# Kernel tuning notes

Measured on AMD Instinct MI355X. Metric: run time of the kernel, lower is better.

## Reference

```python
import jax, jax.numpy as jnp
import numpy as np

N_HEAD, D_K, D_V, EPS = 8, 64, 64, 1e-6


def setup_inputs() -> dict:
    key = jax.random.key(0)
    ks = jax.random.split(key, 7)
    b, n, t, d = 8, 4, 512, 512
    q = jax.random.normal(ks[0], (b, n, t, d), dtype=jnp.float32)
    k = jax.random.normal(ks[1], (b, n, t, d), dtype=jnp.float32)
    v = jax.random.normal(ks[2], (b, n, t, d), dtype=jnp.float32)
    s = 1.0 / np.sqrt(d)
    w_q = jax.random.normal(ks[3], (N_HEAD * D_K, d), dtype=jnp.float32) * s
    w_k = jax.random.normal(ks[4], (N_HEAD * D_K, d), dtype=jnp.float32) * s
    w_v = jax.random.normal(ks[5], (N_HEAD * D_V, d), dtype=jnp.float32) * s
    w_fc = jax.random.normal(ks[6], (d, N_HEAD * D_V), dtype=jnp.float32) * s
    ln_gamma = jnp.ones((d,), dtype=jnp.float32)
    ln_beta = jnp.zeros((d,), dtype=jnp.float32)
    return {"q": q, "k": k, "v": v, "w_q": w_q, "w_k": w_k, "w_v": w_v,
            "w_fc": w_fc, "ln_gamma": ln_gamma, "ln_beta": ln_beta}


def reference(q, k, v, w_q, w_k, w_v, w_fc, ln_gamma, ln_beta):
    b, n, t, d = q.shape
    B = b * n
    qf = q.reshape(B, t, d)
    kf = k.reshape(B, t, d)
    vf = v.reshape(B, t, d)
    residual = qf
    # projections -> [B, H, T, dk/dv]
    Q = jnp.einsum('btd,ed->bte', qf, w_q).reshape(B, t, N_HEAD, D_K).transpose(0, 2, 1, 3)
    K = jnp.einsum('btd,ed->bte', kf, w_k).reshape(B, t, N_HEAD, D_K).transpose(0, 2, 1, 3)
    V = jnp.einsum('btd,ed->bte', vf, w_v).reshape(B, t, N_HEAD, D_V).transpose(0, 2, 1, 3)
    # scaled dot-product attention (scale by sqrt(d_k) of q's last dim)
    scale = 1.0 / jnp.sqrt(jnp.asarray(D_K, dtype=Q.dtype))
    attn = jax.nn.softmax(jnp.einsum('bhqd,bhkd->bhqk', Q * scale, K), axis=-1)
    O = jnp.einsum('bhqk,bhkd->bhqd', attn, V)  # [B, H, T, dv]
    # merge heads, then the original's extra transpose+view (layout scramble)
    x = O.transpose(0, 2, 1, 3).reshape(B, t, N_HEAD * D_V)
    x = jnp.transpose(x, (0, 2, 1)).reshape(B, t, N_HEAD * D_V)
    x = jnp.einsum('bte,de->btd', x, w_fc)
    x = x + residual
    # LayerNorm(eps=1e-6)
    mu = jnp.mean(x, axis=-1, keepdims=True)
    var = jnp.var(x, axis=-1, keepdims=True)
    x = (x - mu) * jax.lax.rsqrt(var + EPS) * ln_gamma + ln_beta
    return x.reshape(b, n, t, d)
```

## Files before the change

### kernel.cpp

```cpp
#include <hip/hip_runtime.h>
#include <hip/hip_bf16.h>
#include <stdint.h>

typedef __attribute__((ext_vector_type(8))) short bf16x8;
typedef __attribute__((ext_vector_type(4))) float f32x4;
typedef unsigned int u32;

#define MFMA16(a,b,c) __builtin_amdgcn_mfma_f32_16x16x32_bf16((a),(b),(c),0,0,0)

__device__ __forceinline__ unsigned short f2bf(float f) {
    unsigned u = __float_as_uint(f);
    u = (u + 0x7FFFu + ((u >> 16) & 1u)) >> 16;
    return (unsigned short)u;
}
__device__ __forceinline__ float bf2f(unsigned short h) {
    return __uint_as_float(((unsigned)h) << 16);
}
__device__ __forceinline__ void gload16(const unsigned short* gp, unsigned short* lp) {
    __builtin_amdgcn_global_load_lds(
        (const __attribute__((address_space(1))) u32*)gp,
        (__attribute__((address_space(3))) u32*)lp, 16, 0, 0);
}
__device__ __forceinline__ int xcd_swz(int bid, int q8) {
    return (bid & 7) * q8 + (bid >> 3);
}


__global__ __launch_bounds__(256) void prep_kernel(
    const float* __restrict__ q, const float* __restrict__ k, const float* __restrict__ v,
    const float* __restrict__ wq, const float* __restrict__ wk, const float* __restrict__ wv,
    const float* __restrict__ wfc,
    unsigned short* __restrict__ Xq, unsigned short* __restrict__ Xk, unsigned short* __restrict__ Xv,
    unsigned short* __restrict__ Wcat)
{
    const long total = 3276800;
    for (long c = (long)blockIdx.x * 256 + threadIdx.x; c < total; c += (long)gridDim.x * 256) {
        const float* src;
        unsigned short* dst;
        long off;
        if (c < 3145728) {
            int t = (int)(c >> 20);
            off = (c & 1048575) * 8;
            src = (t == 0) ? q : (t == 1) ? k : v;
            dst = (t == 0) ? Xq : (t == 1) ? Xk : Xv;
        } else {
            long c2 = c - 3145728;
            int w = (int)(c2 >> 15);
            off = (c2 & 32767) * 8;
            src = (w == 0) ? wq : (w == 1) ? wk : (w == 2) ? wv : wfc;
            dst = Wcat + (long)w * 262144;
        }
        const float4 a = *(const float4*)(src + off);
        const float4 b = *(const float4*)(src + off + 4);
        uint4 pk;
        pk.x = (u32)f2bf(a.x) | ((u32)f2bf(a.y) << 16);
        pk.y = (u32)f2bf(a.z) | ((u32)f2bf(a.w) << 16);
        pk.z = (u32)f2bf(b.x) | ((u32)f2bf(b.y) << 16);
        pk.w = (u32)f2bf(b.z) | ((u32)f2bf(b.w) << 16);
        *(uint4*)(dst + off) = pk;
    }
}

__device__ __forceinline__ void gemm_body(
    const unsigned short* __restrict__ A, const unsigned short* __restrict__ Bm,
    unsigned short* __restrict__ out, int mode, float scale,
    unsigned short* As0, unsigned short* Bs0,
    unsigned short* As1, unsigned short* Bs1,
    int m0, int n0)
{
    const int tid = threadIdx.x, wid = tid >> 6, lane = tid & 63;
    const int wm = wid >> 1, wn = wid & 1;
    const int g = lane >> 4, cc = lane & 15;

    f32x4 acc[4][4];
    #pragma unroll
    for (int a = 0; a < 4; a++)
        #pragma unroll
        for (int b = 0; b < 4; b++)
            acc[a][b] = (f32x4){0.f, 0.f, 0.f, 0.f};

    auto STAGE = [&](unsigned short* As, unsigned short* Bs, int k0) {
        #pragma unroll
        for (int j = 0; j < 4; j++) {
            const int sb = j * 256 + wid * 64;
            const int s = sb + lane;
            const int r = s >> 3;
            const int cd = (s & 7) ^ (r & 7);
            gload16(A  + (size_t)(m0 + r) * 512 + k0 + cd * 8, As + (size_t)sb * 8);
            gload16(Bm + (size_t)(n0 + r) * 512 + k0 + cd * 8, Bs + (size_t)sb * 8);
        }
    };

    STAGE(As0, Bs0, 0);
    __syncthreads();

    #pragma unroll
    for (int t = 0; t < 8; t++) {
        unsigned short* Ac = (t & 1) ? As1 : As0;
        unsigned short* Bc = (t & 1) ? Bs1 : Bs0;
        if (t < 7)
            STAGE((t & 1) ? As0 : As1, (t & 1) ? Bs0 : Bs1, (t + 1) * 64);

        #pragma unroll
        for (int kc = 0; kc < 2; kc++) {
            bf16x8 af[4], bfr[4];
            #pragma unroll
            for (int mf = 0; mf < 4; mf++) {
                const int r = wm * 64 + mf * 16 + cc;
                af[mf] = *(const bf16x8*)(Ac + r * 64 + (((kc * 4 + g) ^ (r & 7)) * 8));
            }
            #pragma unroll
            for (int nf = 0; nf < 4; nf++) {
                const int r = wn * 64 + nf * 16 + cc;
                bfr[nf] = *(const bf16x8*)(Bc + r * 64 + (((kc * 4 + g) ^ (r & 7)) * 8));
            }
            __builtin_amdgcn_s_setprio(1);
            #pragma unroll
            for (int mf = 0; mf < 4; mf++)
                #pragma unroll
                for (int nf = 0; nf < 4; nf++)
                    acc[mf][nf] = MFMA16(af[mf], bfr[nf], acc[mf][nf]);
            __builtin_amdgcn_s_setprio(0);
        }
        __syncthreads();
    }

    #pragma unroll
    for (int mf = 0; mf < 4; mf++) {
        const int rg = m0 + wm * 64 + mf * 16 + g * 4;
        const int t0 = rg & 511, bI = rg >> 9;
        #pragma unroll
        for (int nf = 0; nf < 4; nf++) {
            const int col = n0 + wn * 64 + nf * 16 + cc;
            if (mode == 0) {
                const int h = col >> 6, dd = col & 63;
                const size_t base = ((size_t)((bI * 8 + h) * 512 + t0)) * 64 + dd;
                #pragma unroll
                for (int i = 0; i < 4; i++)
                    out[base + (size_t)i * 64] = f2bf(acc[mf][nf][i] * scale);
            } else if (mode == 1) {
                const int h = col >> 6, dd = col & 63;
                const size_t base = ((size_t)((bI * 8 + h) * 64 + dd)) * 512 + t0;
                uint2 pk;
                pk.x = (u32)f2bf(acc[mf][nf][0]) | ((u32)f2bf(acc[mf][nf][1]) << 16);
                pk.y = (u32)f2bf(acc[mf][nf][2]) | ((u32)f2bf(acc[mf][nf][3]) << 16);
                *(uint2*)(out + base) = pk;
            } else {
                #pragma unroll
                for (int i = 0; i < 4; i++)
                    out[(size_t)(rg + i) * 512 + col] = f2bf(acc[mf][nf][i]);
            }
        }
    }
}

__global__ __launch_bounds__(256) void proj_kernel(
    const unsigned short* __restrict__ Xq, const unsigned short* __restrict__ Xk,
    const unsigned short* __restrict__ Xv, const unsigned short* __restrict__ Wcat,
    unsigned short* __restrict__ Qb, unsigned short* __restrict__ Kb,
    unsigned short* __restrict__ Vt)
{
    __shared__ __align__(16) unsigned short As[2][128 * 64];
    __shared__ __align__(16) unsigned short Bs[2][128 * 64];
    const int work = xcd_swz(blockIdx.x, 192);
    const int x = work & 3, y = (work >> 2) & 127, z = work >> 9;
    const unsigned short* A = (z == 0) ? Xq : (z == 1) ? Xk : Xv;
    const unsigned short* B = Wcat + (size_t)z * 262144;
    unsigned short* out = (z == 0) ? Qb : (z == 1) ? Kb : Vt;
    const int mode = (z == 2) ? 1 : 0;
    const float scale = (z == 0) ? 0.125f : 1.0f;
    gemm_body(A, B, out, mode, scale, As[0], Bs[0], As[1], Bs[1], y * 128, x * 128);
}

__global__ __launch_bounds__(256) void fc_kernel(
    const unsigned short* __restrict__ Os, const unsigned short* __restrict__ Wfc,
    unsigned short* __restrict__ Y)
{
    __shared__ __align__(16) unsigned short As[2][128 * 64];
    __shared__ __align__(16) unsigned short Bs[2][128 * 64];
    const int work = xcd_swz(blockIdx.x, 64);
    const int x = work & 3, y = work >> 2;
    gemm_body(Os, Wfc, Y, 2, 1.0f, As[0], Bs[0], As[1], Bs[1], y * 128, x * 128);
}

__global__ __launch_bounds__(256) void attn_kernel(
    const unsigned short* __restrict__ Qb, const unsigned short* __restrict__ Kb,
    const unsigned short* __restrict__ Vt, unsigned short* __restrict__ Os)
{
    __shared__ __align__(16) unsigned short Ks[64 * 64];
    __shared__ __align__(16) unsigned short Vs[64 * 64];
    __shared__ __align__(16) unsigned short Ps[4 * 32 * 64];

    const int work = xcd_swz(blockIdx.x, 128);
    const int qt = work & 3, bh = work >> 2;
    const int tid = threadIdx.x;
    const int wid = tid >> 6, lane = tid & 63;
    const int g = lane >> 4, cc = lane & 15;

    const unsigned short* Qp = Qb + (size_t)bh * 512 * 64;
    const unsigned short* Kp = Kb + (size_t)bh * 512 * 64;
    const unsigned short* Vp = Vt + (size_t)bh * 64 * 512;

    const int q0 = qt * 128 + wid * 32;

    bf16x8 qf[2][2];
    #pragma unroll
    for (int mf = 0; mf < 2; mf++)
        #pragma unroll
        for (int kb = 0; kb < 2; kb++)
            qf[mf][kb] = *(const bf16x8*)(Qp + (size_t)(q0 + mf * 16 + cc) * 64 + kb * 32 + g * 8);

    f32x4 o[2][4];
    #pragma unroll
    for (int a = 0; a < 2; a++)
        #pragma unroll
        for (int b = 0; b < 4; b++)
            o[a][b] = (f32x4){0.f, 0.f, 0.f, 0.f};
    float lrun[2][4];
    #pragma unroll
    for (int a = 0; a < 2; a++)
        #pragma unroll
        for (int i = 0; i < 4; i++) lrun[a][i] = 0.f;

    const int sb = wid * 64;
    const int s1 = sb + lane, r1 = s1 >> 3, cd1 = (s1 & 7) ^ (r1 & 7);
    const int s2 = sb + 256 + lane, r2 = s2 >> 3, cd2 = (s2 & 7) ^ (r2 & 7);

    for (int kt = 0; kt < 8; kt++) {
        gload16(Kp + (size_t)(kt * 64 + r1) * 64 + cd1 * 8, Ks + (size_t)sb * 8);
        gload16(Kp + (size_t)(kt * 64 + r2) * 64 + cd2 * 8, Ks + (size_t)(sb + 256) * 8);
        gload16(Vp + (size_t)r1 * 512 + kt * 64 + cd1 * 8, Vs + (size_t)sb * 8);
        gload16(Vp + (size_t)r2 * 512 + kt * 64 + cd2 * 8, Vs + (size_t)(sb + 256) * 8);
        __syncthreads();

        f32x4 s[2][4];
        #pragma unroll
        for (int a = 0; a < 2; a++)
            #pragma unroll
            for (int b = 0; b < 4; b++)
                s[a][b] = (f32x4){0.f, 0.f, 0.f, 0.f};
        __builtin_amdgcn_s_setprio(1);
        #pragma unroll
        for (int nf = 0; nf < 4; nf++) {
            const int r = nf * 16 + cc;
            #pragma unroll
            for (int kb = 0; kb < 2; kb++) {
                bf16x8 kf = *(const bf16x8*)(Ks + r * 64 + (((kb * 4 + g) ^ (r & 7)) * 8));
                s[0][nf] = MFMA16(qf[0][kb], kf, s[0][nf]);
                s[1][nf] = MFMA16(qf[1][kb], kf, s[1][nf]);
            }
        }
        __builtin_amdgcn_s_setprio(0);

        unsigned short* Pw = Ps + wid * 32 * 64;
        #pragma unroll
        for (int mf = 0; mf < 2; mf++)
            #pragma unroll
            for (int i = 0; i < 4; i++) {
                float lacc = 0.f;
                #pragma unroll
                for (int nf = 0; nf < 4; nf++) {
                    float p = __expf(s[mf][nf][i]);
                    s[mf][nf][i] = p;
                    lacc += p;
                }
                lrun[mf][i] += lacc;
            }

        #pragma unroll
        for (int mf = 0; mf < 2; mf++)
            #pragma unroll
            for (int nf = 0; nf < 4; nf++) {
                const int c = nf * 16 + cc, csl = c >> 3, cin = c & 7;
                #pragma unroll
                for (int i = 0; i < 4; i++) {
                    const int row = mf * 16 + g * 4 + i;
                    Pw[row * 64 + ((csl ^ (row & 7)) * 8) + cin] = f2bf(s[mf][nf][i]);
                }
            }

        __builtin_amdgcn_s_setprio(1);
        #pragma unroll
        for (int kc = 0; kc < 2; kc++) {
            bf16x8 pa[2], vb[4];
            #pragma unroll
            for (int mf = 0; mf < 2; mf++) {
                const int r = mf * 16 + cc;
                pa[mf] = *(const bf16x8*)(Pw + r * 64 + (((kc * 4 + g) ^ (r & 7)) * 8));
            }
            #pragma unroll
            for (int vf = 0; vf < 4; vf++) {
                const int r = vf * 16 + cc;
                vb[vf] = *(const bf16x8*)(Vs + r * 64 + (((kc * 4 + g) ^ (r & 7)) * 8));
            }
            #pragma unroll
            for (int mf = 0; mf < 2; mf++)
                #pragma unroll
                for (int vf = 0; vf < 4; vf++)
                    o[mf][vf] = MFMA16(pa[mf], vb[vf], o[mf][vf]);
        }
        __builtin_amdgcn_s_setprio(0);
        __syncthreads();
    }

    const int b = bh >> 3, h = bh & 7;
    #pragma unroll
    for (int mf = 0; mf < 2; mf++) {
        int tq0 = q0 + mf * 16 + g * 4;
        float inv[4];
        #pragma unroll
        for (int i = 0; i < 4; i++) {
            float l = lrun[mf][i];
            #pragma unroll
            for (int d = 1; d < 16; d <<= 1) l += __shfl_xor(l, d);
            inv[i] = 1.0f / l;
        }
        #pragma unroll
        for (int vf = 0; vf < 4; vf++) {
            int dv = vf * 16 + cc;
            uint2 pk;
            pk.x = (u32)f2bf(o[mf][vf][0] * inv[0]) | ((u32)f2bf(o[mf][vf][1] * inv[1]) << 16);
            pk.y = (u32)f2bf(o[mf][vf][2] * inv[2]) | ((u32)f2bf(o[mf][vf][3] * inv[3]) << 16);
            size_t base = ((size_t)b * 512 + h * 64 + dv) * 512 + tq0;
            *(uint2*)(Os + base) = pk;
        }
    }
}

__global__ __launch_bounds__(256) void ln_kernel(
    const unsigned short* __restrict__ y, const unsigned short* __restrict__ residb,
    const float* __restrict__ residf,
    const float* __restrict__ gamma, const float* __restrict__ beta,
    float* __restrict__ out, int use_bf16_resid)
{
    const int wid = threadIdx.x >> 6, lane = threadIdx.x & 63;
    const int row = blockIdx.x * 4 + wid;
    const unsigned short* yr = y + (size_t)row * 512;

    const bf16x8 yv = *(const bf16x8*)(yr + lane * 8);
    float x[8];
    if (use_bf16_resid) {
        const bf16x8 rv = *(const bf16x8*)(residb + (size_t)row * 512 + lane * 8);
        #pragma unroll
        for (int j = 0; j < 8; j++)
            x[j] = bf2f((unsigned short)yv[j]) + bf2f((unsigned short)rv[j]);
    } else {
        const float* rr = residf + (size_t)row * 512;
        const float4 r0 = *(const float4*)(rr + lane * 8);
        const float4 r1 = *(const float4*)(rr + lane * 8 + 4);
        x[0] = bf2f((unsigned short)yv[0]) + r0.x;
        x[1] = bf2f((unsigned short)yv[1]) + r0.y;
        x[2] = bf2f((unsigned short)yv[2]) + r0.z;
        x[3] = bf2f((unsigned short)yv[3]) + r0.w;
        x[4] = bf2f((unsigned short)yv[4]) + r1.x;
        x[5] = bf2f((unsigned short)yv[5]) + r1.y;
        x[6] = bf2f((unsigned short)yv[6]) + r1.z;
        x[7] = bf2f((unsigned short)yv[7]) + r1.w;
    }

    float s = 0.f, sq = 0.f;
    #pragma unroll
    for (int j = 0; j < 8; j++) { s += x[j]; sq += x[j] * x[j]; }
    #pragma unroll
    for (int d = 1; d < 64; d <<= 1) {
        s += __shfl_xor(s, d);
        sq += __shfl_xor(sq, d);
    }
    const float mu = s * (1.0f / 512.0f);
    const float var = sq * (1.0f / 512.0f) - mu * mu;
    const float rs = rsqrtf(var + 1e-6f);

    #pragma unroll
    for (int j = 0; j < 2; j++) {
        const int colb = lane * 8 + j * 4;
        const float4 gg = *(const float4*)(gamma + colb);
        const float4 bb = *(const float4*)(beta + colb);
        float4 ov;
        ov.x = (x[j * 4 + 0] - mu) * rs * gg.x + bb.x;
        ov.y = (x[j * 4 + 1] - mu) * rs * gg.y + bb.y;
        ov.z = (x[j * 4 + 2] - mu) * rs * gg.z + bb.z;
        ov.w = (x[j * 4 + 3] - mu) * rs * gg.w + bb.w;
        *(float4*)(out + (size_t)row * 512 + colb) = ov;
    }
}

extern "C" void kernel_launch(void* const* d_in, const int* in_sizes, int n_in,
                              void* d_out, int out_size, void* d_ws, size_t ws_size,
                              hipStream_t stream) {
    const float* q     = (const float*)d_in[0];
    const float* k     = (const float*)d_in[1];
    const float* v     = (const float*)d_in[2];
    const float* wq    = (const float*)d_in[3];
    const float* wk    = (const float*)d_in[4];
    const float* wv    = (const float*)d_in[5];
    const float* wfc   = (const float*)d_in[6];
    const float* gamma = (const float*)d_in[7];
    const float* beta  = (const float*)d_in[8];
    float* out = (float*)d_out;

    char* ws = (char*)d_ws;
    const size_t SEG = 16777216;
    const bool big = ws_size >= 6 * SEG + 2097152;

    unsigned short *Xq, *Xk, *Xv, *Qb, *Kb, *Vt, *Os, *Y, *Wcat;
    if (big) {
        Xq = (unsigned short*)(ws);
        Xk = (unsigned short*)(ws + SEG);
        Xv = (unsigned short*)(ws + 2 * SEG);
        Qb = (unsigned short*)(ws + 3 * SEG);
        Kb = (unsigned short*)(ws + 4 * SEG);
        Vt = (unsigned short*)(ws + 5 * SEG);
        Wcat = (unsigned short*)(ws + 6 * SEG);
        Os = Xk; Y = Xv;
    } else {
        Xq = (unsigned short*)(ws);
        Xk = (unsigned short*)(ws + SEG);
        Xv = (unsigned short*)(ws + 2 * SEG);
        Qb = (unsigned short*)(ws + 3 * SEG);
        Vt = (unsigned short*)(ws + 4 * SEG);
        Wcat = (unsigned short*)(ws + 5 * SEG);
        Kb = Xq; Os = Xk; Y = Xv;
    }

    prep_kernel<<<2048, 256, 0, stream>>>(q, k, v, wq, wk, wv, wfc, Xq, Xk, Xv, Wcat);
    proj_kernel<<<1536, 256, 0, stream>>>(Xq, Xk, Xv, Wcat, Qb, Kb, Vt);
    attn_kernel<<<1024, 256, 0, stream>>>(Qb, Kb, Vt, Os);
    fc_kernel<<<512, 256, 0, stream>>>(Os, Wcat + 786432, Y);
    ln_kernel<<<4096, 256, 0, stream>>>(Y, big ? Xq : (unsigned short*)nullptr, q,
                                        gamma, beta, out, big ? 1 : 0);
}
```

Measured before the change: 129.8 us.

## Fuse fp32-to-bf16 activation conversion into projection GEMM A-tile loads

The separate prep pass that converted q/k/v to bf16 in workspace is removed. The projection GEMM now reads fp32 activations straight into registers, converts them and writes the tile to LDS after the MFMA work, overlapping with the asynchronous LDS load of B. Only the weights are still pre-converted. This drops a full write and reread of the bf16 activations. In exchange, the proj kernel reads fp32 A tiles (twice the bytes per tile), each A tile is re-read and re-converted by all four column blocks, and register pressure rises.

Measured after the change: 125.8 us. -3.1%, faster.

```diff
diff --git a/kernel.cpp b/kernel.cpp
--- a/kernel.cpp
+++ b/kernel.cpp
@@ -26,48 +26,43 @@
 }
 
 
-__global__ __launch_bounds__(256) void prep_kernel(
-    const float* __restrict__ q, const float* __restrict__ k, const float* __restrict__ v,
+__global__ __launch_bounds__(256) void prep_w(
     const float* __restrict__ wq, const float* __restrict__ wk, const float* __restrict__ wv,
-    const float* __restrict__ wfc,
-    unsigned short* __restrict__ Xq, unsigned short* __restrict__ Xk, unsigned short* __restrict__ Xv,
-    unsigned short* __restrict__ Wcat)
+    const float* __restrict__ wfc, unsigned short* __restrict__ Wcat)
 {
-    const long total = 3276800;
-    for (long c = (long)blockIdx.x * 256 + threadIdx.x; c < total; c += (long)gridDim.x * 256) {
-        const float* src;
-        unsigned short* dst;
-        long off;
-        if (c < 3145728) {
-            int t = (int)(c >> 20);
-            off = (c & 1048575) * 8;
-            src = (t == 0) ? q : (t == 1) ? k : v;
-            dst = (t == 0) ? Xq : (t == 1) ? Xk : Xv;
-        } else {
-            long c2 = c - 3145728;
-            int w = (int)(c2 >> 15);
-            off = (c2 & 32767) * 8;
-            src = (w == 0) ? wq : (w == 1) ? wk : (w == 2) ? wv : wfc;
-            dst = Wcat + (long)w * 262144;
-        }
-        const float4 a = *(const float4*)(src + off);
-        const float4 b = *(const float4*)(src + off + 4);
-        uint4 pk;
-        pk.x = (u32)f2bf(a.x) | ((u32)f2bf(a.y) << 16);
-        pk.y = (u32)f2bf(a.z) | ((u32)f2bf(a.w) << 16);
-        pk.z = (u32)f2bf(b.x) | ((u32)f2bf(b.y) << 16);
-        pk.w = (u32)f2bf(b.z) | ((u32)f2bf(b.w) << 16);
-        *(uint4*)(dst + off) = pk;
-    }
-}
-
-__device__ __forceinline__ void gemm_body(
-    const unsigned short* __restrict__ A, const unsigned short* __restrict__ Bm,
-    unsigned short* __restrict__ out, int mode, float scale,
-    unsigned short* As0, unsigned short* Bs0,
-    unsigned short* As1, unsigned short* Bs1,
-    int m0, int n0)
+    const int c = blockIdx.x * 256 + threadIdx.x;
+    const int w = c >> 15;
+    const long off = (long)(c & 32767) * 8;
+    const float* src = (w == 0) ? wq : (w == 1) ? wk : (w == 2) ? wv : wfc;
+    unsigned short* dst = Wcat + (long)w * 262144;
+    const float4 a = *(const float4*)(src + off);
+    const float4 b = *(const float4*)(src + off + 4);
+    uint4 pk;
+    pk.x = (u32)f2bf(a.x) | ((u32)f2bf(a.y) << 16);
+    pk.y = (u32)f2bf(a.z) | ((u32)f2bf(a.w) << 16);
+    pk.z = (u32)f2bf(b.x) | ((u32)f2bf(b.y) << 16);
+    pk.w = (u32)f2bf(b.z) | ((u32)f2bf(b.w) << 16);
+    *(uint4*)(dst + off) = pk;
+}
+
+__global__ __launch_bounds__(256) void proj_kernel(
+    const float* __restrict__ qf, const float* __restrict__ kf, const float* __restrict__ vf,
+    const unsigned short* __restrict__ Wcat,
+    unsigned short* __restrict__ Qb, unsigned short* __restrict__ Kb,
+    unsigned short* __restrict__ Vt)
 {
+    __shared__ __align__(16) unsigned short As[2][128 * 64];
+    __shared__ __align__(16) unsigned short Bs[2][128 * 64];
+
+    const int work = xcd_swz(blockIdx.x, 192);
+    const int x = work & 3, y = (work >> 2) & 127, z = work >> 9;
+    const float* Af = (z == 0) ? qf : (z == 1) ? kf : vf;
+    const unsigned short* Bm = Wcat + (size_t)z * 262144;
+    unsigned short* out = (z == 0) ? Qb : (z == 1) ? Kb : Vt;
+    const int mode = (z == 2) ? 1 : 0;
+    const float scale = (z == 0) ? 0.125f : 1.0f;
+    const int m0 = y * 128, n0 = x * 128;
+
     const int tid = threadIdx.x, wid = tid >> 6, lane = tid & 63;
     const int wm = wid >> 1, wn = wid & 1;
     const int g = lane >> 4, cc = lane & 15;
@@ -79,27 +74,53 @@
         for (int b = 0; b < 4; b++)
             acc[a][b] = (f32x4){0.f, 0.f, 0.f, 0.f};
 
-    auto STAGE = [&](unsigned short* As, unsigned short* Bs, int k0) {
+    int sslot[4], srow[4], scd[4];
+    #pragma unroll
+    for (int j = 0; j < 4; j++) {
+        const int s = j * 256 + wid * 64 + lane;
+        sslot[j] = s; srow[j] = s >> 3; scd[j] = (s & 7) ^ ((s >> 3) & 7);
+    }
+
+    float4 ra[8];
+    auto LOADA = [&](int k0) {
+        #pragma unroll
+        for (int j = 0; j < 4; j++) {
+            const float* src = Af + (size_t)(m0 + srow[j]) * 512 + k0 + scd[j] * 8;
+            ra[2 * j]     = *(const float4*)src;
+            ra[2 * j + 1] = *(const float4*)(src + 4);
+        }
+    };
+    auto WRITEA = [&](unsigned short* Asb) {
+        #pragma unroll
+        for (int j = 0; j < 4; j++) {
+            uint4 pk;
+            pk.x = (u32)f2bf(ra[2 * j].x)     | ((u32)f2bf(ra[2 * j].y) << 16);
+            pk.y = (u32)f2bf(ra[2 * j].z)     | ((u32)f2bf(ra[2 * j].w) << 16);
+            pk.z = (u32)f2bf(ra[2 * j + 1].x) | ((u32)f2bf(ra[2 * j + 1].y) << 16);
+            pk.w = (u32)f2bf(ra[2 * j + 1].z) | ((u32)f2bf(ra[2 * j + 1].w) << 16);
+            *(uint4*)(Asb + (size_t)sslot[j] * 8) = pk;
+        }
+    };
+    auto STAGEB = [&](unsigned short* Bsb, int k0) {
         #pragma unroll
         for (int j = 0; j < 4; j++) {
             const int sb = j * 256 + wid * 64;
-            const int s = sb + lane;
-            const int r = s >> 3;
-            const int cd = (s & 7) ^ (r & 7);
-            gload16(A  + (size_t)(m0 + r) * 512 + k0 + cd * 8, As + (size_t)sb * 8);
-            gload16(Bm + (size_t)(n0 + r) * 512 + k0 + cd * 8, Bs + (size_t)sb * 8);
+            gload16(Bm + (size_t)(n0 + srow[j]) * 512 + k0 + scd[j] * 8,
+                    Bsb + (size_t)sb * 8);
         }
     };
 
-    STAGE(As0, Bs0, 0);
+    LOADA(0); STAGEB(Bs[0], 0); WRITEA(As[0]);
     __syncthreads();
 
     #pragma unroll
     for (int t = 0; t < 8; t++) {
-        unsigned short* Ac = (t & 1) ? As1 : As0;
-        unsigned short* Bc = (t & 1) ? Bs1 : Bs0;
-        if (t < 7)
-            STAGE((t & 1) ? As0 : As1, (t & 1) ? Bs0 : Bs1, (t + 1) * 64);
+        unsigned short* Ac = As[t & 1];
+        unsigned short* Bc = Bs[t & 1];
+        if (t < 7) {
+            LOADA((t + 1) * 64);
+            STAGEB(Bs[(t + 1) & 1], (t + 1) * 64);
+        }
 
         #pragma unroll
         for (int kc = 0; kc < 2; kc++) {
@@ -122,6 +143,7 @@
                     acc[mf][nf] = MFMA16(af[mf], bfr[nf], acc[mf][nf]);
             __builtin_amdgcn_s_setprio(0);
         }
+        if (t < 7) WRITEA(As[(t + 1) & 1]);
         __syncthreads();
     }
 
@@ -132,44 +154,21 @@
         #pragma unroll
         for (int nf = 0; nf < 4; nf++) {
             const int col = n0 + wn * 64 + nf * 16 + cc;
+            const int h = col >> 6, dd = col & 63;
             if (mode == 0) {
-                const int h = col >> 6, dd = col & 63;
                 const size_t base = ((size_t)((bI * 8 + h) * 512 + t0)) * 64 + dd;
                 #pragma unroll
                 for (int i = 0; i < 4; i++)
                     out[base + (size_t)i * 64] = f2bf(acc[mf][nf][i] * scale);
-            } else if (mode == 1) {
-                const int h = col >> 6, dd = col & 63;
+            } else {
                 const size_t base = ((size_t)((bI * 8 + h) * 64 + dd)) * 512 + t0;
                 uint2 pk;
                 pk.x = (u32)f2bf(acc[mf][nf][0]) | ((u32)f2bf(acc[mf][nf][1]) << 16);
                 pk.y = (u32)f2bf(acc[mf][nf][2]) | ((u32)f2bf(acc[mf][nf][3]) << 16);
                 *(uint2*)(out + base) = pk;
-            } else {
-                #pragma unroll
-                for (int i = 0; i < 4; i++)
-                    out[(size_t)(rg + i) * 512 + col] = f2bf(acc[mf][nf][i]);
-            }
-        }
-    }
-}
-
-__global__ __launch_bounds__(256) void proj_kernel(
-    const unsigned short* __restrict__ Xq, const unsigned short* __restrict__ Xk,
-    const unsigned short* __restrict__ Xv, const unsigned short* __restrict__ Wcat,
-    unsigned short* __restrict__ Qb, unsigned short* __restrict__ Kb,
-    unsigned short* __restrict__ Vt)
-{
-    __shared__ __align__(16) unsigned short As[2][128 * 64];
-    __shared__ __align__(16) unsigned short Bs[2][128 * 64];
-    const int work = xcd_swz(blockIdx.x, 192);
-    const int x = work & 3, y = (work >> 2) & 127, z = work >> 9;
-    const unsigned short* A = (z == 0) ? Xq : (z == 1) ? Xk : Xv;
-    const unsigned short* B = Wcat + (size_t)z * 262144;
-    unsigned short* out = (z == 0) ? Qb : (z == 1) ? Kb : Vt;
-    const int mode = (z == 2) ? 1 : 0;
-    const float scale = (z == 0) ? 0.125f : 1.0f;
-    gemm_body(A, B, out, mode, scale, As[0], Bs[0], As[1], Bs[1], y * 128, x * 128);
+            }
+        }
+    }
 }
 
 __global__ __launch_bounds__(256) void fc_kernel(
@@ -179,8 +178,75 @@
     __shared__ __align__(16) unsigned short As[2][128 * 64];
     __shared__ __align__(16) unsigned short Bs[2][128 * 64];
     const int work = xcd_swz(blockIdx.x, 64);
-    const int x = work & 3, y = work >> 2;
-    gemm_body(Os, Wfc, Y, 2, 1.0f, As[0], Bs[0], As[1], Bs[1], y * 128, x * 128);
+    const int n0 = (work & 3) * 128, m0 = (work >> 2) * 128;
+
+    const int tid = threadIdx.x, wid = tid >> 6, lane = tid & 63;
+    const int wm = wid >> 1, wn = wid & 1;
+    const int g = lane >> 4, cc = lane & 15;
+
+    f32x4 acc[4][4];
+    #pragma unroll
+    for (int a = 0; a < 4; a++)
+        #pragma unroll
+        for (int b = 0; b < 4; b++)
+            acc[a][b] = (f32x4){0.f, 0.f, 0.f, 0.f};
+
+    auto STAGE = [&](unsigned short* Asb, unsigned short* Bsb, int k0) {
+        #pragma unroll
+        for (int j = 0; j < 4; j++) {
+            const int sb = j * 256 + wid * 64;
+            const int s = sb + lane;
+            const int r = s >> 3;
+            const int cd = (s & 7) ^ (r & 7);
+            gload16(Os  + (size_t)(m0 + r) * 512 + k0 + cd * 8, Asb + (size_t)sb * 8);
+            gload16(Wfc + (size_t)(n0 + r) * 512 + k0 + cd * 8, Bsb + (size_t)sb * 8);
+        }
+    };
+
+    STAGE(As[0], Bs[0], 0);
+    __syncthreads();
+
+    #pragma unroll
+    for (int t = 0; t < 8; t++) {
+        unsigned short* Ac = As[t & 1];
+        unsigned short* Bc = Bs[t & 1];
+        if (t < 7) STAGE(As[(t + 1) & 1], Bs[(t + 1) & 1], (t + 1) * 64);
+
+        #pragma unroll
+        for (int kc = 0; kc < 2; kc++) {
+            bf16x8 af[4], bfr[4];
+            #pragma unroll
+            for (int mf = 0; mf < 4; mf++) {
+                const int r = wm * 64 + mf * 16 + cc;
+                af[mf] = *(const bf16x8*)(Ac + r * 64 + (((kc * 4 + g) ^ (r & 7)) * 8));
+            }
+            #pragma unroll
+            for (int nf = 0; nf < 4; nf++) {
+                const int r = wn * 64 + nf * 16 + cc;
+                bfr[nf] = *(const bf16x8*)(Bc + r * 64 + (((kc * 4 + g) ^ (r & 7)) * 8));
+            }
+            __builtin_amdgcn_s_setprio(1);
+            #pragma unroll
+            for (int mf = 0; mf < 4; mf++)
+                #pragma unroll
+                for (int nf = 0; nf < 4; nf++)
+                    acc[mf][nf] = MFMA16(af[mf], bfr[nf], acc[mf][nf]);
+            __builtin_amdgcn_s_setprio(0);
+        }
+        __syncthreads();
+    }
+
+    #pragma unroll
+    for (int mf = 0; mf < 4; mf++) {
+        const int rg = m0 + wm * 64 + mf * 16 + g * 4;
+        #pragma unroll
+        for (int nf = 0; nf < 4; nf++) {
+            const int col = n0 + wn * 64 + nf * 16 + cc;
+            #pragma unroll
+            for (int i = 0; i < 4; i++)
+                Y[(size_t)(rg + i) * 512 + col] = f2bf(acc[mf][nf][i]);
+        }
+    }
 }
 
 __global__ __launch_bounds__(256) void attn_kernel(
@@ -328,35 +394,27 @@
 }
 
 __global__ __launch_bounds__(256) void ln_kernel(
-    const unsigned short* __restrict__ y, const unsigned short* __restrict__ residb,
-    const float* __restrict__ residf,
+    const unsigned short* __restrict__ y, const float* __restrict__ resid,
     const float* __restrict__ gamma, const float* __restrict__ beta,
-    float* __restrict__ out, int use_bf16_resid)
+    float* __restrict__ out)
 {
     const int wid = threadIdx.x >> 6, lane = threadIdx.x & 63;
     const int row = blockIdx.x * 4 + wid;
     const unsigned short* yr = y + (size_t)row * 512;
+    const float* rr = resid + (size_t)row * 512;
 
     const bf16x8 yv = *(const bf16x8*)(yr + lane * 8);
+    const float4 r0 = *(const float4*)(rr + lane * 8);
+    const float4 r1 = *(const float4*)(rr + lane * 8 + 4);
     float x[8];
-    if (use_bf16_resid) {
-        const bf16x8 rv = *(const bf16x8*)(residb + (size_t)row * 512 + lane * 8);
-        #pragma unroll
-        for (int j = 0; j < 8; j++)
-            x[j] = bf2f((unsigned short)yv[j]) + bf2f((unsigned short)rv[j]);
-    } else {
-        const float* rr = residf + (size_t)row * 512;
-        const float4 r0 = *(const float4*)(rr + lane * 8);
-        const float4 r1 = *(const float4*)(rr + lane * 8 + 4);
-        x[0] = bf2f((unsigned short)yv[0]) + r0.x;
-        x[1] = bf2f((unsigned short)yv[1]) + r0.y;
-        x[2] = bf2f((unsigned short)yv[2]) + r0.z;
-        x[3] = bf2f((unsigned short)yv[3]) + r0.w;
-        x[4] = bf2f((unsigned short)yv[4]) + r1.x;
-        x[5] = bf2f((unsigned short)yv[5]) + r1.y;
-        x[6] = bf2f((unsigned short)yv[6]) + r1.z;
-        x[7] = bf2f((unsigned short)yv[7]) + r1.w;
-    }
+    x[0] = bf2f((unsigned short)yv[0]) + r0.x;
+    x[1] = bf2f((unsigned short)yv[1]) + r0.y;
+    x[2] = bf2f((unsigned short)yv[2]) + r0.z;
+    x[3] = bf2f((unsigned short)yv[3]) + r0.w;
+    x[4] = bf2f((unsigned short)yv[4]) + r1.x;
+    x[5] = bf2f((unsigned short)yv[5]) + r1.y;
+    x[6] = bf2f((unsigned short)yv[6]) + r1.z;
+    x[7] = bf2f((unsigned short)yv[7]) + r1.w;
 
     float s = 0.f, sq = 0.f;
     #pragma unroll
@@ -400,32 +458,16 @@
 
     char* ws = (char*)d_ws;
     const size_t SEG = 16777216;
-    const bool big = ws_size >= 6 * SEG + 2097152;
-
-    unsigned short *Xq, *Xk, *Xv, *Qb, *Kb, *Vt, *Os, *Y, *Wcat;
-    if (big) {
-        Xq = (unsigned short*)(ws);
-        Xk = (unsigned short*)(ws + SEG);
-        Xv = (unsigned short*)(ws + 2 * SEG);
-        Qb = (unsigned short*)(ws + 3 * SEG);
-        Kb = (unsigned short*)(ws + 4 * SEG);
-        Vt = (unsigned short*)(ws + 5 * SEG);
-        Wcat = (unsigned short*)(ws + 6 * SEG);
-        Os = Xk; Y = Xv;
-    } else {
-        Xq = (unsigned short*)(ws);
-        Xk = (unsigned short*)(ws + SEG);
-        Xv = (unsigned short*)(ws + 2 * SEG);
-        Qb = (unsigned short*)(ws + 3 * SEG);
-        Vt = (unsigned short*)(ws + 4 * SEG);
-        Wcat = (unsigned short*)(ws + 5 * SEG);
-        Kb = Xq; Os = Xk; Y = Xv;
-    }
-
-    prep_kernel<<<2048, 256, 0, stream>>>(q, k, v, wq, wk, wv, wfc, Xq, Xk, Xv, Wcat);
-    proj_kernel<<<1536, 256, 0, stream>>>(Xq, Xk, Xv, Wcat, Qb, Kb, Vt);
+    unsigned short* Qb   = (unsigned short*)(ws);
+    unsigned short* Kb   = (unsigned short*)(ws + SEG);
+    unsigned short* Vt   = (unsigned short*)(ws + 2 * SEG);
+    unsigned short* Os   = (unsigned short*)(ws + 3 * SEG);
+    unsigned short* Y    = (unsigned short*)(ws + 4 * SEG);
+    unsigned short* Wcat = (unsigned short*)(ws + 5 * SEG);
+
+    prep_w<<<512, 256, 0, stream>>>(wq, wk, wv, wfc, Wcat);
+    proj_kernel<<<1536, 256, 0, stream>>>(q, k, v, Wcat, Qb, Kb, Vt);
     attn_kernel<<<1024, 256, 0, stream>>>(Qb, Kb, Vt, Os);
     fc_kernel<<<512, 256, 0, stream>>>(Os, Wcat + 786432, Y);
-    ln_kernel<<<4096, 256, 0, stream>>>(Y, big ? Xq : (unsigned short*)nullptr, q,
-                                        gamma, beta, out, big ? 1 : 0);
-}
+    ln_kernel<<<4096, 256, 0, stream>>>(Y, q, gamma, beta, out);
+}
```
